# Performance work log

Measured on AMD Instinct MI355X. Metric: run time of the kernel, lower is better.

Reference implementation:

```python
import jax, jax.numpy as jnp
import numpy as np
from jax import lax

DT = jnp.float32
P_DIM = 21
G_VEC = jnp.array([0.0, 0.0, -9.80665], dtype=DT)
# process-noise diag: (omega, acc, b_omega, b_acc, Rot_c_i, t_c_i) x3 each (NumPyIEKF.Parameters defaults)
Q_DIAG = jnp.array([1e-3] * 3 + [1e-2] * 3 + [6e-9] * 3 + [2e-4] * 3 + [1e-9] * 3 + [1e-9] * 3, dtype=DT)
COV_ROT0, COV_V0 = 1e-3, 1e-1
COV_B_OMEGA0, COV_B_ACC0 = 6e-3, 4e-3
COV_ROT_C_I0, COV_T_C_I0 = 1e-6, 5e-3


def _skew(x):
    z = jnp.zeros((), x.dtype)
    return jnp.stack([
        jnp.stack([z, -x[2], x[1]]),
        jnp.stack([x[2], z, -x[0]]),
        jnp.stack([-x[1], x[0], z]),
    ])


def _so3exp(phi):
    # SO(3) exponential (Rodrigues), safe at phi ~ 0 via double-where.
    I3 = jnp.eye(3, dtype=phi.dtype)
    sq = jnp.dot(phi, phi)
    small = sq < 1e-16
    angle = jnp.sqrt(jnp.where(small, 1.0, sq))
    axis = phi / angle
    s, c = jnp.sin(angle), jnp.cos(angle)
    R = c * I3 + (1.0 - c) * jnp.outer(axis, axis) + s * _skew(axis)
    return jnp.where(small, I3 + _skew(phi), R)


def _sen3exp(xi):
    # SE_2(3) exponential: xi is 9-vector [phi, dv_raw, dp_raw]; returns (dR, x) with x[:,0]=dv, x[:,1]=dp.
    phi = xi[:3]
    I3 = jnp.eye(3, dtype=xi.dtype)
    sq = jnp.dot(phi, phi)
    small = sq < 1e-16
    angle = jnp.sqrt(jnp.where(small, 1.0, sq))
    axis = phi / angle
    s, c = jnp.sin(angle), jnp.cos(angle)
    sk = _skew(axis)
    outer = jnp.outer(axis, axis)
    sa = s / angle
    J = sa * I3 + (1.0 - sa) * outer + ((1.0 - c) / angle) * sk
    R = c * I3 + (1.0 - c) * outer + s * sk
    J = jnp.where(small, I3 + 0.5 * _skew(phi), J)
    R = jnp.where(small, I3 + _skew(phi), R)
    x = J @ xi[3:].reshape(2, 3).T  # (3,2)
    return R, x


def _from_rpy(roll, pitch, yaw):
    cr, sr = jnp.cos(roll), jnp.sin(roll)
    cp, sp = jnp.cos(pitch), jnp.sin(pitch)
    cy, sy = jnp.cos(yaw), jnp.sin(yaw)
    z = jnp.zeros((), roll.dtype)
    o = jnp.ones((), roll.dtype)
    rx = jnp.stack([jnp.stack([o, z, z]), jnp.stack([z, cr, -sr]), jnp.stack([z, sr, cr])])
    ry = jnp.stack([jnp.stack([cp, z, sp]), jnp.stack([z, o, z]), jnp.stack([-sp, z, cp])])
    rz = jnp.stack([jnp.stack([cy, -sy, z]), jnp.stack([sy, cy, z]), jnp.stack([z, z, o])])
    return rz @ ry @ rx


def _propagate_cov(P, Rot, v, p, u, dt):
    I3 = jnp.eye(3, dtype=P.dtype)
    v_skew_rot = _skew(v) @ Rot
    p_skew_rot = _skew(p) @ Rot
    F = jnp.zeros((P_DIM, P_DIM), P.dtype)
    F = F.at[3:6, :3].set(_skew(G_VEC))
    F = F.at[6:9, 3:6].set(I3)
    F = F.at[3:6, 12:15].set(-Rot)
    F = F.at[:3, 9:12].set(-Rot)
    F = F.at[3:6, 9:12].set(-v_skew_rot)
    F = F.at[6:9, 9:12].set(-p_skew_rot)
    G = jnp.zeros((P_DIM, 18), P.dtype)
    G = G.at[:3, :3].set(Rot).at[3:6, :3].set(v_skew_rot).at[6:9, :3].set(p_skew_rot)
    G = G.at[3:6, 3:6].set(Rot)
    G = G.at[9:12, 6:9].set(I3).at[12:15, 9:12].set(I3).at[15:18, 12:15].set(I3).at[18:21, 15:18].set(I3)
    F = F * dt
    G = G * dt
    F2 = F @ F
    Phi = jnp.eye(P_DIM, dtype=P.dtype) + F + 0.5 * F2 + (1.0 / 6.0) * (F2 @ F)
    return Phi @ (P + (G * Q_DIAG) @ G.T) @ Phi.T


def _step(carry, inp):
    Rot, v, p, b_omega, b_acc, Rot_c_i, t_c_i, P = carry
    u, dt, mcov = inp
    # ---- propagate ----
    acc = Rot @ (u[3:6] - b_acc) + G_VEC
    v_n = v + acc * dt
    p_n = p + v * dt + 0.5 * acc * dt * dt
    Rot_n = Rot @ _so3exp((u[:3] - b_omega) * dt)
    P_n = _propagate_cov(P, Rot, v, p, u, dt)
    # ---- update: zero lateral/vertical body-velocity pseudo-measurement ----
    Rot_body = Rot_n @ Rot_c_i
    v_imu = Rot_n.T @ v_n
    omega = u[:3] - b_omega
    v_body = Rot_c_i.T @ v_imu + _skew(t_c_i) @ omega
    H = jnp.zeros((2, P_DIM), P.dtype)
    H = H.at[:, 3:6].set(Rot_body.T[1:])
    H = H.at[:, 15:18].set((Rot_c_i.T @ _skew(v_imu))[1:])
    H = H.at[:, 9:12].set(_skew(t_c_i)[1:])
    H = H.at[:, 18:21].set(-_skew(omega)[1:])
    r = -v_body[1:]
    Rm = jnp.diag(mcov)
    S = H @ P_n @ H.T + Rm  # (2,2)
    K = jnp.linalg.solve(S, H @ P_n.T).T  # K = P H^T S^{-1}, (21,2)
    dx = K @ r
    dR, dxi = _sen3exp(dx[:9])
    Rot_u = dR @ Rot_n
    v_u = dR @ v_n + dxi[:, 0]
    p_u = dR @ p_n + dxi[:, 1]
    b_omega_u = b_omega + dx[9:12]
    b_acc_u = b_acc + dx[12:15]
    Rot_c_i_u = _so3exp(dx[15:18]) @ Rot_c_i
    t_c_i_u = t_c_i + dx[18:21]
    I_KH = jnp.eye(P_DIM, dtype=P.dtype) - K @ H
    P_u = I_KH @ P_n @ I_KH.T + K @ Rm @ K.T
    P_u = 0.5 * (P_u + P_u.T)
    carry = (Rot_u, v_u, p_u, b_omega_u, b_acc_u, Rot_c_i_u, t_c_i_u, P_u)
    return carry, (Rot_u, v_u, p_u, b_omega_u, b_acc_u, Rot_c_i_u, t_c_i_u)


def _run_filter(t, u, mc, v_mes, ang0, remat=False):
    dt = t[1:] - t[:-1]
    dtype = u.dtype
    Rot0 = _from_rpy(ang0[0], ang0[1], ang0[2]).astype(dtype)
    v0 = v_mes[0]
    z3 = jnp.zeros(3, dtype)
    I3 = jnp.eye(3, dtype=dtype)
    p_diag = jnp.array(
        [COV_ROT0, COV_ROT0, 0.0, COV_V0, COV_V0, 0.0, 0.0, 0.0, 0.0]
        + [COV_B_OMEGA0] * 3 + [COV_B_ACC0] * 3 + [COV_ROT_C_I0] * 3 + [COV_T_C_I0] * 3,
        dtype=dtype,
    )
    P0 = jnp.diag(p_diag)
    step = jax.checkpoint(_step) if remat else _step
    carry0 = (Rot0, v0, z3, z3, z3, I3, z3, P0)
    _, traj = lax.scan(step, carry0, (u[1:], dt, mc[1:]))
    first = (Rot0, v0, z3, z3, z3, I3, z3)
    return tuple(jnp.concatenate([f[None], tr], axis=0) for f, tr in zip(first, traj))


def setup_inputs() -> dict:
    key = jax.random.key(0)
    N = 40000  # ~6.7 min of 100 Hz IMU
    k1, k2, k3, k4, k5, k6 = jax.random.split(key, 6)
    t = jnp.arange(N, dtype=DT) * 0.01
    gyro = 0.05 * jax.random.normal(k1, (N, 3), dtype=DT)
    accm = jnp.array([0.0, 0.0, 9.80665], dtype=DT) + 0.1 * jax.random.normal(k2, (N, 3), dtype=DT)
    u = jnp.concatenate([gyro, accm], axis=1)
    measurements_covs = 0.01 + jax.random.uniform(k3, (N, 2), dtype=DT)
    v_mes = jax.random.normal(k4, (N, 3), dtype=DT)
    p_mes = jax.random.normal(k5, (N, 3), dtype=DT)
    ang0 = 0.1 * jax.random.normal(k6, (3,), dtype=DT)
    return {"t": t, "u": u, "measurements_covs": measurements_covs, "v_mes": v_mes,
            "p_mes": p_mes, "ang0": ang0, "N": N}


def reference(t, u, measurements_covs, v_mes, p_mes, ang0, N):
    # p_mes is accepted by run()/init_run() but unused (parity with source).
    return _run_filter(t[:N], u[:N], measurements_covs[:N], v_mes[:N], ang0)
```

## Files before the change

kernel.cpp:

```cpp
#include <hip/hip_runtime.h>
#include <math.h>


#define GRAV 9.80665f
#define P24 24
#define PC  12
#define Q0c 0.001f
#define Q1c 0.01f

#define WSYNC() asm volatile("s_waitcnt lgkmcnt(0)" ::: "memory")

__device__ __forceinline__ float sel3f(int r, float a, float b, float c) {
    return (r == 0) ? a : ((r == 1) ? b : c);
}

__device__ __forceinline__ void m3mul_dev(const float* A, const float* B, float* C) {
#pragma unroll
    for (int i = 0; i < 3; ++i) {
#pragma unroll
        for (int j = 0; j < 3; ++j) {
            C[i*3+j] = A[i*3+0]*B[j] + A[i*3+1]*B[3+j] + A[i*3+2]*B[6+j];
        }
    }
}

__device__ __forceinline__ void so3exp_dev(float p0, float p1, float p2, float* R) {
    float sq = p0*p0 + p1*p1 + p2*p2;
    if (sq < 1e-16f) {
        R[0]=1.f;  R[1]=-p2;  R[2]=p1;
        R[3]=p2;   R[4]=1.f;  R[5]=-p0;
        R[6]=-p1;  R[7]=p0;   R[8]=1.f;
    } else {
        float ang = sqrtf(sq);
        float ax=p0/ang, ay=p1/ang, az=p2/ang;
        float s=sinf(ang), c=cosf(ang), o=1.f-c;
        R[0]=c+o*ax*ax;    R[1]=o*ax*ay-s*az; R[2]=o*ax*az+s*ay;
        R[3]=o*ay*ax+s*az; R[4]=c+o*ay*ay;    R[5]=o*ay*az-s*ax;
        R[6]=o*az*ax-s*ay; R[7]=o*az*ay+s*ax; R[8]=c+o*az*az;
    }
}

#define STORE_TRAJ(NIDX)                                                        \
    do {                                                                        \
        if (l < 33) {                                                           \
            float val = Rot[0];                                                 \
            if (l==1) val=Rot[1];  if (l==2) val=Rot[2];                        \
            if (l==3) val=Rot[3];  if (l==4) val=Rot[4];                        \
            if (l==5) val=Rot[5];  if (l==6) val=Rot[6];                        \
            if (l==7) val=Rot[7];  if (l==8) val=Rot[8];                        \
            if (l==9)  val=vv[0];  if (l==10) val=vv[1];  if (l==11) val=vv[2]; \
            if (l==12) val=pp[0];  if (l==13) val=pp[1];  if (l==14) val=pp[2]; \
            if (l==15) val=bw[0];  if (l==16) val=bw[1];  if (l==17) val=bw[2]; \
            if (l==18) val=ba[0];  if (l==19) val=ba[1];  if (l==20) val=ba[2]; \
            if (l==21) val=Rci[0]; if (l==22) val=Rci[1]; if (l==23) val=Rci[2];\
            if (l==24) val=Rci[3]; if (l==25) val=Rci[4]; if (l==26) val=Rci[5];\
            if (l==27) val=Rci[6]; if (l==28) val=Rci[7]; if (l==29) val=Rci[8];\
            if (l==30) val=tci[0]; if (l==31) val=tci[1]; if (l==32) val=tci[2];\
            out[ob + os_ * (NIDX) + orr] = val;                                 \
        }                                                                       \
    } while (0)

__global__ __launch_bounds__(64, 1)
void iekf_scan_kernel(const float* __restrict__ t,
                      const float* __restrict__ u,
                      const float* __restrict__ mc,
                      const float* __restrict__ v_mes,
                      const float* __restrict__ ang0,
                      float* __restrict__ out,
                      const int N)
{
    __shared__ __align__(16) float sRows[10*4];
    __shared__ __align__(16) float sPhiC[21*PC];
    __shared__ __align__(16) float sAT [22*P24];
    __shared__ __align__(16) float sT1 [22*P24];
    __shared__ __align__(16) float sPn [22*P24];
    __shared__ __align__(16) float sPnT[22*P24];
    __shared__ __align__(16) float sHpack[21*4];
    __shared__ __align__(16) float sKpack[21*4];
    __shared__ __align__(16) float sdx[24];

    const int l = (int)threadIdx.x;

    int ei[7], ej[7], wro[7], wco[7];
    bool ev[7];
#pragma unroll
    for (int q = 0; q < 7; ++q) {
        const int e = 64*q + l;
        const bool v = (e < 441);
        const int ii = e / 21;
        const int jj = e - ii*21;
        ev[q] = v;
        ei[q] = v ? ii : 20;
        ej[q] = v ? jj : 20;
        wro[q] = (v ? ii : 21)*P24 + ej[q];
        wco[q] = (v ? jj : 21)*P24 + ei[q];
    }

    float Rot[9], vv[3], pp[3], bw[3], ba[3], Rci[9], tci[3];
    {
        const float roll = ang0[0], pitch = ang0[1], yaw = ang0[2];
        const float cr = cosf(roll),  srl = sinf(roll);
        const float cp = cosf(pitch), spt = sinf(pitch);
        const float cy = cosf(yaw),   syw = sinf(yaw);
        float rx[9] = {1.f,0.f,0.f, 0.f,cr,-srl, 0.f,srl,cr};
        float ry[9] = {cp,0.f,spt, 0.f,1.f,0.f, -spt,0.f,cp};
        float rz[9] = {cy,-syw,0.f, syw,cy,0.f, 0.f,0.f,1.f};
        float tm[9]; m3mul_dev(rz, ry, tm);
        m3mul_dev(tm, rx, Rot);
        vv[0]=v_mes[0]; vv[1]=v_mes[1]; vv[2]=v_mes[2];
#pragma unroll
        for (int c=0;c<3;c++){ pp[c]=0.f; bw[c]=0.f; ba[c]=0.f; tci[c]=0.f; }
        Rci[0]=1.f;Rci[1]=0.f;Rci[2]=0.f;Rci[3]=0.f;Rci[4]=1.f;Rci[5]=0.f;
        Rci[6]=0.f;Rci[7]=0.f;Rci[8]=1.f;
    }

    float Preg[7];
#pragma unroll
    for (int q = 0; q < 7; ++q) {
        float pd = 0.f;
        if (ev[q] && ei[q] == ej[q]) {
            const int ii = ei[q];
            if (ii==0 || ii==1)        pd = 0.001f;
            else if (ii==3 || ii==4)   pd = 0.1f;
            else if (ii>=9  && ii<12)  pd = 0.006f;
            else if (ii>=12 && ii<15)  pd = 0.004f;
            else if (ii>=15 && ii<18)  pd = 1e-6f;
            else if (ii>=18)           pd = 0.005f;
        }
        Preg[q] = pd;
    }

    int ob=0, os_=0, orr=0;
    if (l<33) {
        if (l<9)       { ob = 0;    os_ = 9; orr = l;    }
        else if (l<12) { ob = 9*N;  os_ = 3; orr = l-9;  }
        else if (l<15) { ob = 12*N; os_ = 3; orr = l-12; }
        else if (l<18) { ob = 15*N; os_ = 3; orr = l-15; }
        else if (l<21) { ob = 18*N; os_ = 3; orr = l-18; }
        else if (l<30) { ob = 21*N; os_ = 9; orr = l-21; }
        else           { ob = 30*N; os_ = 3; orr = l-30; }
    }

    STORE_TRAJ(0);

    float t_cur = t[0];

    float tn_c = t[1];
    float uc0,uc1,uc2,uc3,uc4,uc5;
    { const float* un = u + 6; uc0=un[0]; uc1=un[1]; uc2=un[2]; uc3=un[3]; uc4=un[4]; uc5=un[5]; }
    float mcc0 = mc[2], mcc1 = mc[3];

    for (int n = 0; n < N-1; ++n) {
        const int np2 = (n+2 < N) ? (n+2) : (N-1);
        const float tn_n = t[np2];
        float un0,un1,un2,un3,un4,un5;
        { const float* un = u + (size_t)np2*6; un0=un[0]; un1=un[1]; un2=un[2]; un3=un[3]; un4=un[4]; un5=un[5]; }
        const float mcn0 = mc[2*np2], mcn1 = mc[2*np2+1];

        const float dt  = tn_c - t_cur;
        const float dt2 = dt*dt;
        const float u0=uc0,u1=uc1,u2=uc2,u3=uc3,u4=uc4,u5=uc5;
        const float mcv0=mcc0, mcv1=mcc1;

        float Rot_n[9], v_n[3], p_n[3], om[3], M1[9], M2[9];
        om[0]=u0-bw[0]; om[1]=u1-bw[1]; om[2]=u2-bw[2];
        {
            const float ai0=u3-ba[0], ai1=u4-ba[1], ai2=u5-ba[2];
            const float ac0 = Rot[0]*ai0 + Rot[1]*ai1 + Rot[2]*ai2;
            const float ac1 = Rot[3]*ai0 + Rot[4]*ai1 + Rot[5]*ai2;
            const float ac2 = Rot[6]*ai0 + Rot[7]*ai1 + Rot[8]*ai2 - GRAV;
            v_n[0]=vv[0]+ac0*dt; v_n[1]=vv[1]+ac1*dt; v_n[2]=vv[2]+ac2*dt;
            p_n[0]=pp[0]+vv[0]*dt+0.5f*ac0*dt2;
            p_n[1]=pp[1]+vv[1]*dt+0.5f*ac1*dt2;
            p_n[2]=pp[2]+vv[2]*dt+0.5f*ac2*dt2;
            float E[9]; so3exp_dev(om[0]*dt, om[1]*dt, om[2]*dt, E);
            m3mul_dev(Rot, E, Rot_n);
        }
#pragma unroll
        for (int c=0;c<3;c++) {
            M1[0+c] = -vv[2]*Rot[3+c] + vv[1]*Rot[6+c];
            M1[3+c] =  vv[2]*Rot[0+c] - vv[0]*Rot[6+c];
            M1[6+c] = -vv[1]*Rot[0+c] + vv[0]*Rot[3+c];
            M2[0+c] = -pp[2]*Rot[3+c] + pp[1]*Rot[6+c];
            M2[3+c] =  pp[2]*Rot[0+c] - pp[0]*Rot[6+c];
            M2[6+c] = -pp[1]*Rot[0+c] + pp[0]*Rot[3+c];
        }
        const float hdt2 = 0.5f*dt2;
        const float sdt3 = dt*dt2*(1.0f/6.0f);
        const float dtg = dt*GRAV, hg = hdt2*GRAV;

        if (l < 27) {
            const int ri = l/3, c = l - 3*ri;
            const int rr = (ri<3) ? ri : ((ri<6) ? ri-3 : ri-6);
            const float rotv = sel3f(c, sel3f(rr,Rot[0],Rot[3],Rot[6]),
                                        sel3f(rr,Rot[1],Rot[4],Rot[7]),
                                        sel3f(rr,Rot[2],Rot[5],Rot[8]));
            const float m1v  = sel3f(c, sel3f(rr,M1[0],M1[3],M1[6]),
                                        sel3f(rr,M1[1],M1[4],M1[7]),
                                        sel3f(rr,M1[2],M1[5],M1[8]));
            const float m2v  = sel3f(c, sel3f(rr,M2[0],M2[3],M2[6]),
                                        sel3f(rr,M2[1],M2[4],M2[7]),
                                        sel3f(rr,M2[2],M2[5],M2[8]));
            sRows[ri*4 + c] = (ri<3) ? rotv : ((ri<6) ? m1v : m2v);
        }
        if (l < 21) {
            const int j = l, br = j/3, r = j - 3*br;
            float cf[12];
#pragma unroll
            for (int c=0;c<3;c++) {
                const float m0r = sel3f(r, Rot[0+c], Rot[3+c], Rot[6+c]);
                const float m1r = sel3f(r, M1[0+c], M1[3+c], M1[6+c]);
                const float m2r = sel3f(r, M2[0+c], M2[3+c], M2[6+c]);
                const float sgm = sel3f(r, GRAV*Rot[3+c], -GRAV*Rot[0+c], 0.f);
                cf[0+c] = (br==0) ? (-dt*m0r)
                        : (br==1) ? (-dt*m1r - hdt2*sgm)
                        : (br==2) ? (-dt*m2r - hdt2*m1r - sdt3*sgm) : 0.f;
                cf[3+c] = (br==1) ? (-dt*m0r) : (br==2) ? (-hdt2*m0r) : 0.f;
                cf[8+c] = (br==2 && r==c) ? dt : 0.f;
            }
            cf[6] = (br==1) ? ((r==1)? -dtg : 0.f) : (br==2) ? ((r==1)? -hg : 0.f) : 0.f;
            cf[7] = (br==1) ? ((r==0)?  dtg : 0.f) : (br==2) ? ((r==0)?  hg : 0.f) : 0.f;
            cf[11] = 0.f;
            float4 w0; w0.x=cf[0]; w0.y=cf[1]; w0.z=cf[2]; w0.w=cf[3];
            float4 w1; w1.x=cf[4]; w1.y=cf[5]; w1.z=cf[6]; w1.w=cf[7];
            float4 w2; w2.x=cf[8]; w2.y=cf[9]; w2.z=cf[10]; w2.w=cf[11];
            *(float4*)&sPhiC[j*PC+0] = w0;
            *(float4*)&sPhiC[j*PC+4] = w1;
            *(float4*)&sPhiC[j*PC+8] = w2;
        }

        float H0_3,H0_4,H0_5,H1_3,H1_4,H1_5,H0_9,H0_10,H0_11,H1_9,H1_10,H1_11;
        float H0_15,H0_16,H0_17,H1_15,H1_16,H1_17,H0_18,H0_19,H0_20,H1_18,H1_19,H1_20;
        float r0s, r1s;
        {
            float Rb[9]; m3mul_dev(Rot_n, Rci, Rb);
            const float vi0 = Rot_n[0]*v_n[0] + Rot_n[3]*v_n[1] + Rot_n[6]*v_n[2];
            const float vi1 = Rot_n[1]*v_n[0] + Rot_n[4]*v_n[1] + Rot_n[7]*v_n[2];
            const float vi2 = Rot_n[2]*v_n[0] + Rot_n[5]*v_n[1] + Rot_n[8]*v_n[2];
            H0_3 = Rb[1]; H0_4 = Rb[4]; H0_5 = Rb[7];
            H1_3 = Rb[2]; H1_4 = Rb[5]; H1_5 = Rb[8];
            H0_9 = tci[2]; H0_10 = 0.f; H0_11 = -tci[0];
            H1_9 = -tci[1]; H1_10 = tci[0]; H1_11 = 0.f;
            H0_15 =  Rci[4]*vi2 - Rci[7]*vi1;
            H0_16 = -Rci[1]*vi2 + Rci[7]*vi0;
            H0_17 =  Rci[1]*vi1 - Rci[4]*vi0;
            H1_15 =  Rci[5]*vi2 - Rci[8]*vi1;
            H1_16 = -Rci[2]*vi2 + Rci[8]*vi0;
            H1_17 =  Rci[2]*vi1 - Rci[5]*vi0;
            H0_18 = -om[2]; H0_19 = 0.f; H0_20 = om[0];
            H1_18 = om[1];  H1_19 = -om[0]; H1_20 = 0.f;
            const float vb1 = Rci[1]*vi0 + Rci[4]*vi1 + Rci[7]*vi2 + (tci[2]*om[0] - tci[0]*om[2]);
            const float vb2 = Rci[2]*vi0 + Rci[5]*vi1 + Rci[8]*vi2 + (tci[0]*om[1] - tci[1]*om[0]);
            r0s = -vb1; r1s = -vb2;
        }
        WSYNC();

        float Areg[7];
#pragma unroll
        for (int q = 0; q < 7; ++q) {
            float Wij;
            if (q <= 2) {
                const bool gqv = (ei[q] < 9) && (ej[q] < 9);
                const int ra_r = (ei[q] < 9) ? ei[q] : 9;
                const int rb_r = (ej[q] < 9) ? ej[q] : 9;
                const float4 ra = *(const float4*)&sRows[ra_r*4];
                const float4 rb = *(const float4*)&sRows[rb_r*4];
                float w = dt2*Q0c*(ra.x*rb.x + ra.y*rb.y + ra.z*rb.z);
                const int ri = ei[q]-3, rj = ej[q]-3;
                const float ra0=sel3f(ri,Rot[0],Rot[3],Rot[6]), ra1=sel3f(ri,Rot[1],Rot[4],Rot[7]), ra2=sel3f(ri,Rot[2],Rot[5],Rot[8]);
                const float rb0=sel3f(rj,Rot[0],Rot[3],Rot[6]), rb1=sel3f(rj,Rot[1],Rot[4],Rot[7]), rb2=sel3f(rj,Rot[2],Rot[5],Rot[8]);
                const bool q1v = (ri>=0 && ri<3 && rj>=0 && rj<3);
                const float w2 = w + dt2*Q1c*(ra0*rb0 + ra1*rb1 + ra2*rb2);
                w = q1v ? w2 : w;
                Wij = gqv ? w : 0.f;
            } else {
                const bool dg = ev[q] && (ei[q] == ej[q]);
                const float qd = (ei[q]<12) ? 6e-9f : (ei[q]<15) ? 2e-4f : 1e-9f;
                Wij = dg ? dt2*qd : 0.f;
            }
            Areg[q] = Preg[q] + Wij;
            sAT[wco[q]] = Areg[q];
        }
        WSYNC();

        float T1reg[7];
#pragma unroll
        for (int q = 0; q < 7; ++q) {
            float tv = Areg[q];
            if (q <= 2) {
                const int co = ei[q]*PC;
                const float4 c0 = *(const float4*)&sPhiC[co];
                const float4 c1 = *(const float4*)&sPhiC[co+4];
                const float4 c2 = *(const float4*)&sPhiC[co+8];
                const int ro = ej[q]*P24;
                const float4 a0 = *(const float4*)&sAT[ro];
                const float4 a1 = *(const float4*)&sAT[ro+4];
                const float4 a2 = *(const float4*)&sAT[ro+8];
                const float4 a3 = *(const float4*)&sAT[ro+12];
                tv += c1.z*a0.x;
                tv += c1.w*a0.y;
                tv += c2.x*a0.w;
                tv += c2.y*a1.x;
                tv += c2.z*a1.y;
                tv += c0.x*a2.y;
                tv += c0.y*a2.z;
                tv += c0.z*a2.w;
                tv += c0.w*a3.x;
                tv += c1.x*a3.y;
                tv += c1.y*a3.z;
            }
            T1reg[q] = tv;
            sT1[wro[q]] = tv;
        }
        WSYNC();

        float Pnreg[7];
#pragma unroll
        for (int q = 0; q < 7; ++q) {
            const int co = ej[q]*PC;
            const float4 c0 = *(const float4*)&sPhiC[co];
            const float4 c1 = *(const float4*)&sPhiC[co+4];
            const float4 c2 = *(const float4*)&sPhiC[co+8];
            const int ro = ei[q]*P24;
            const float4 t0 = *(const float4*)&sT1[ro];
            const float4 t1 = *(const float4*)&sT1[ro+4];
            const float4 t2 = *(const float4*)&sT1[ro+8];
            const float4 t3 = *(const float4*)&sT1[ro+12];
            float pv = T1reg[q];
            pv += c1.z*t0.x;
            pv += c1.w*t0.y;
            pv += c2.x*t0.w;
            pv += c2.y*t1.x;
            pv += c2.z*t1.y;
            pv += c0.x*t2.y;
            pv += c0.y*t2.z;
            pv += c0.z*t2.w;
            pv += c0.w*t3.x;
            pv += c1.x*t3.y;
            pv += c1.y*t3.z;
            Pnreg[q] = pv;
            sPn [wro[q]] = pv;
            sPnT[wco[q]] = pv;
        }
        WSYNC();

        {
            const int a  = l / 21;
            const int jj = (l < 42) ? (l - 21*a) : 0;
            const int ro = jj*P24;
            const float4 p0 = *(const float4*)&sPnT[ro];
            const float4 p1 = *(const float4*)&sPnT[ro+4];
            const float4 p2 = *(const float4*)&sPnT[ro+8];
            const float4 p3 = *(const float4*)&sPnT[ro+12];
            const float4 p4 = *(const float4*)&sPnT[ro+16];
            const float4 p5 = *(const float4*)&sPnT[ro+20];
            const float4 q0 = *(const float4*)&sPn[ro];
            const float4 q1 = *(const float4*)&sPn[ro+4];
            const float4 q2 = *(const float4*)&sPn[ro+8];
            const float4 q3 = *(const float4*)&sPn[ro+12];
            const float4 q4 = *(const float4*)&sPn[ro+16];
            const float4 q5 = *(const float4*)&sPn[ro+20];
            const bool a0v = (a == 0);
            const float h3  = a0v ? H0_3  : H1_3,  h4  = a0v ? H0_4  : H1_4,  h5  = a0v ? H0_5  : H1_5;
            const float h9  = a0v ? H0_9  : H1_9,  h10 = a0v ? H0_10 : H1_10, h11 = a0v ? H0_11 : H1_11;
            const float h15 = a0v ? H0_15 : H1_15, h16 = a0v ? H0_16 : H1_16, h17 = a0v ? H0_17 : H1_17;
            const float h18 = a0v ? H0_18 : H1_18, h19 = a0v ? H0_19 : H1_19, h20 = a0v ? H0_20 : H1_20;
            float hp = 0.f;
            hp += h3*p0.w;  hp += h4*p1.x;  hp += h5*p1.y;
            hp += h9*p2.y;  hp += h10*p2.z; hp += h11*p2.w;
            hp += h15*p3.w; hp += h16*p4.x; hp += h17*p4.y;
            hp += h18*p4.z; hp += h19*p4.w; hp += h20*p5.x;
            float ht = 0.f;
            ht += h3*q0.w;  ht += h4*q1.x;  ht += h5*q1.y;
            ht += h9*q2.y;  ht += h10*q2.z; ht += h11*q2.w;
            ht += h15*q3.w; ht += h16*q4.x; ht += h17*q4.y;
            ht += h18*q4.z; ht += h19*q4.w; ht += h20*q5.x;
            if (l < 42) {
                sHpack[jj*4 + a]     = hp;
                sHpack[jj*4 + 2 + a] = ht;
            }
        }
        WSYNC();

        {
            const float4 v3  = *(const float4*)&sHpack[3*4];
            const float4 v4  = *(const float4*)&sHpack[4*4];
            const float4 v5  = *(const float4*)&sHpack[5*4];
            const float4 v9  = *(const float4*)&sHpack[9*4];
            const float4 v10 = *(const float4*)&sHpack[10*4];
            const float4 v11 = *(const float4*)&sHpack[11*4];
            const float4 v15 = *(const float4*)&sHpack[15*4];
            const float4 v16 = *(const float4*)&sHpack[16*4];
            const float4 v17 = *(const float4*)&sHpack[17*4];
            const float4 v18 = *(const float4*)&sHpack[18*4];
            const float4 v19 = *(const float4*)&sHpack[19*4];
            const float4 v20 = *(const float4*)&sHpack[20*4];
            float S00 = 0.f, S01 = 0.f, S10 = 0.f, S11 = 0.f;
            S00 += v3.x*H0_3;  S00 += v4.x*H0_4;  S00 += v5.x*H0_5;
            S00 += v9.x*H0_9;  S00 += v10.x*H0_10; S00 += v11.x*H0_11;
            S00 += v15.x*H0_15; S00 += v16.x*H0_16; S00 += v17.x*H0_17;
            S00 += v18.x*H0_18; S00 += v19.x*H0_19; S00 += v20.x*H0_20;
            S01 += v3.x*H1_3;  S01 += v4.x*H1_4;  S01 += v5.x*H1_5;
            S01 += v9.x*H1_9;  S01 += v10.x*H1_10; S01 += v11.x*H1_11;
            S01 += v15.x*H1_15; S01 += v16.x*H1_16; S01 += v17.x*H1_17;
            S01 += v18.x*H1_18; S01 += v19.x*H1_19; S01 += v20.x*H1_20;
            S10 += v3.y*H0_3;  S10 += v4.y*H0_4;  S10 += v5.y*H0_5;
            S10 += v9.y*H0_9;  S10 += v10.y*H0_10; S10 += v11.y*H0_11;
            S10 += v15.y*H0_15; S10 += v16.y*H0_16; S10 += v17.y*H0_17;
            S10 += v18.y*H0_18; S10 += v19.y*H0_19; S10 += v20.y*H0_20;
            S11 += v3.y*H1_3;  S11 += v4.y*H1_4;  S11 += v5.y*H1_5;
            S11 += v9.y*H1_9;  S11 += v10.y*H1_10; S11 += v11.y*H1_11;
            S11 += v15.y*H1_15; S11 += v16.y*H1_16; S11 += v17.y*H1_17;
            S11 += v18.y*H1_18; S11 += v19.y*H1_19; S11 += v20.y*H1_20;
            S00 += mcv0; S11 += mcv1;
            if (l < 21) {
                const float4 own = *(const float4*)&sHpack[l*4];
                const float b0 = own.z, b1 = own.w;
                float x0, x1;
                if (fabsf(S00) >= fabsf(S10)) {
                    const float fac = S10/S00;
                    x1 = (b1 - fac*b0) / (S11 - fac*S01);
                    x0 = (b0 - S01*x1) / S00;
                } else {
                    const float fac = S00/S10;
                    x1 = (b0 - fac*b1) / (S01 - fac*S11);
                    x0 = (b1 - S11*x1) / S10;
                }
                float4 kp; kp.x = x0; kp.y = x1;
                kp.z = S00*x0 + S01*x1;
                kp.w = S10*x0 + S11*x1;
                *(float4*)&sKpack[l*4] = kp;
                sdx[l] = x0*r0s + x1*r1s;
            }
        }
        WSYNC();

#pragma unroll
        for (int q = 0; q < 7; ++q) {
            const float4 Ki = *(const float4*)&sKpack[ei[q]*4];
            const float4 Kj = *(const float4*)&sKpack[ej[q]*4];
            const float4 Hi = *(const float4*)&sHpack[ei[q]*4];
            const float4 Hj = *(const float4*)&sHpack[ej[q]*4];
            const float pn_ji = sPnT[ei[q]*P24 + ej[q]];
            const float puij = Pnreg[q] - (Ki.x*Hj.x + Ki.y*Hj.y) - (Hi.z*Kj.x + Hi.w*Kj.y)
                                        + (Ki.x*Kj.z + Ki.y*Kj.w);
            const float puji = pn_ji   - (Kj.x*Hi.x + Kj.y*Hi.y) - (Hj.z*Ki.x + Hj.w*Ki.y)
                                        + (Kj.x*Ki.z + Kj.y*Ki.w);
            const float pu = 0.5f*(puij + puji);
            Preg[q] = ev[q] ? pu : Preg[q];
        }
        {
            float dxr[21];
#pragma unroll
            for (int q2=0;q2<6;q2++){
                const float4 x = *(const float4*)(&sdx[4*q2]);
                dxr[4*q2] = x.x;
                if (4*q2+1 < 21) dxr[4*q2+1] = x.y;
                if (4*q2+2 < 21) dxr[4*q2+2] = x.z;
                if (4*q2+3 < 21) dxr[4*q2+3] = x.w;
            }
            float dR[9], Jm[9];
            const float q0 = dxr[0], q1 = dxr[1], q2 = dxr[2];
            const float sq = q0*q0 + q1*q1 + q2*q2;
            if (sq < 1e-16f) {
                dR[0]=1.f; dR[1]=-q2; dR[2]=q1;
                dR[3]=q2;  dR[4]=1.f; dR[5]=-q0;
                dR[6]=-q1; dR[7]=q0;  dR[8]=1.f;
                Jm[0]=1.f;      Jm[1]=-0.5f*q2; Jm[2]=0.5f*q1;
                Jm[3]=0.5f*q2;  Jm[4]=1.f;      Jm[5]=-0.5f*q0;
                Jm[6]=-0.5f*q1; Jm[7]=0.5f*q0;  Jm[8]=1.f;
            } else {
                const float ang = sqrtf(sq);
                const float ax=q0/ang, ay=q1/ang, az=q2/ang;
                const float s=sinf(ang), c=cosf(ang), o=1.f-c;
                dR[0]=c+o*ax*ax;    dR[1]=o*ax*ay-s*az; dR[2]=o*ax*az+s*ay;
                dR[3]=o*ay*ax+s*az; dR[4]=c+o*ay*ay;    dR[5]=o*ay*az-s*ax;
                dR[6]=o*az*ax-s*ay; dR[7]=o*az*ay+s*ax; dR[8]=c+o*az*az;
                const float sa  = s/ang;
                const float osa = 1.f - sa;
                const float tt  = o/ang;
                Jm[0]=sa+osa*ax*ax;    Jm[1]=osa*ax*ay-tt*az; Jm[2]=osa*ax*az+tt*ay;
                Jm[3]=osa*ay*ax+tt*az; Jm[4]=sa+osa*ay*ay;    Jm[5]=osa*ay*az-tt*ax;
                Jm[6]=osa*az*ax-tt*ay; Jm[7]=osa*az*ay+tt*ax; Jm[8]=sa+osa*az*az;
            }
            float nR[9]; m3mul_dev(dR, Rot_n, nR);
#pragma unroll
            for (int c=0;c<9;c++) Rot[c] = nR[c];
            const float dv0 = Jm[0]*dxr[3] + Jm[1]*dxr[4] + Jm[2]*dxr[5];
            const float dv1 = Jm[3]*dxr[3] + Jm[4]*dxr[4] + Jm[5]*dxr[5];
            const float dv2 = Jm[6]*dxr[3] + Jm[7]*dxr[4] + Jm[8]*dxr[5];
            const float dp0 = Jm[0]*dxr[6] + Jm[1]*dxr[7] + Jm[2]*dxr[8];
            const float dp1 = Jm[3]*dxr[6] + Jm[4]*dxr[7] + Jm[5]*dxr[8];
            const float dp2 = Jm[6]*dxr[6] + Jm[7]*dxr[7] + Jm[8]*dxr[8];
            const float nv0 = dR[0]*v_n[0] + dR[1]*v_n[1] + dR[2]*v_n[2] + dv0;
            const float nv1 = dR[3]*v_n[0] + dR[4]*v_n[1] + dR[5]*v_n[2] + dv1;
            const float nv2 = dR[6]*v_n[0] + dR[7]*v_n[1] + dR[8]*v_n[2] + dv2;
            const float np0 = dR[0]*p_n[0] + dR[1]*p_n[1] + dR[2]*p_n[2] + dp0;
            const float np1 = dR[3]*p_n[0] + dR[4]*p_n[1] + dR[5]*p_n[2] + dp1;
            const float np2v= dR[6]*p_n[0] + dR[7]*p_n[1] + dR[8]*p_n[2] + dp2;
            vv[0]=nv0; vv[1]=nv1; vv[2]=nv2;
            pp[0]=np0; pp[1]=np1; pp[2]=np2v;
            bw[0]+=dxr[9];  bw[1]+=dxr[10]; bw[2]+=dxr[11];
            ba[0]+=dxr[12]; ba[1]+=dxr[13]; ba[2]+=dxr[14];
            float E2[9]; so3exp_dev(dxr[15], dxr[16], dxr[17], E2);
            float nRc[9]; m3mul_dev(E2, Rci, nRc);
#pragma unroll
            for (int c=0;c<9;c++) Rci[c] = nRc[c];
            tci[0]+=dxr[18]; tci[1]+=dxr[19]; tci[2]+=dxr[20];
        }
        STORE_TRAJ(n+1);

        t_cur = tn_c;
        tn_c  = tn_n;
        uc0=un0; uc1=un1; uc2=un2; uc3=un3; uc4=un4; uc5=un5;
        mcc0=mcn0; mcc1=mcn1;
    }
}

extern "C" void kernel_launch(void* const* d_in, const int* in_sizes, int n_in,
                              void* d_out, int out_size, void* d_ws, size_t ws_size,
                              hipStream_t stream) {
    const float* t     = (const float*)d_in[0];
    const float* u     = (const float*)d_in[1];
    const float* mc    = (const float*)d_in[2];
    const float* v_mes = (const float*)d_in[3];
    const float* ang0  = (const float*)d_in[5];
    float* out = (float*)d_out;
    const int N = in_sizes[0];
    (void)d_ws; (void)ws_size; (void)n_in; (void)out_size;
    iekf_scan_kernel<<<1, 64, 0, stream>>>(t, u, mc, v_mes, ang0, out, N);
}
```

Before: 202.4 ms.

## Switch covariance update to per-thread column ownership in registers

Instead of distributing the 441 covariance entries across 64 threads in 7-element chunks, each of the first 21 threads now owns a full column of P in registers. Phi coefficients are computed inline rather than staged through shared memory, which removes several shared buffers and one barrier stage. Each thread also solves the 2x2 innovation system redundantly, so there is no separate K broadcast pass. The trade-off is that only 21 of 64 lanes do useful work, and each thread needs many more registers for its column arrays and coefficient tables.

```diff
diff --git a/kernel.cpp b/kernel.cpp
--- a/kernel.cpp
+++ b/kernel.cpp
@@ -3,8 +3,7 @@
 
 
 #define GRAV 9.80665f
-#define P24 24
-#define PC  12
+#define PIT 36
 #define Q0c 0.001f
 #define Q1c 0.01f
 
@@ -69,32 +68,17 @@
                       float* __restrict__ out,
                       const int N)
 {
-    __shared__ __align__(16) float sRows[10*4];
-    __shared__ __align__(16) float sPhiC[21*PC];
-    __shared__ __align__(16) float sAT [22*P24];
-    __shared__ __align__(16) float sT1 [22*P24];
-    __shared__ __align__(16) float sPn [22*P24];
-    __shared__ __align__(16) float sPnT[22*P24];
-    __shared__ __align__(16) float sHpack[21*4];
-    __shared__ __align__(16) float sKpack[21*4];
+    __shared__ __align__(16) float sT1[21*PIT];
+    __shared__ __align__(16) float sPT[21*PIT];
+    __shared__ __align__(16) float sHK[21*4];
+    __shared__ __align__(16) float sKK[21*4];
     __shared__ __align__(16) float sdx[24];
 
     const int l = (int)threadIdx.x;
-
-    int ei[7], ej[7], wro[7], wco[7];
-    bool ev[7];
-#pragma unroll
-    for (int q = 0; q < 7; ++q) {
-        const int e = 64*q + l;
-        const bool v = (e < 441);
-        const int ii = e / 21;
-        const int jj = e - ii*21;
-        ev[q] = v;
-        ei[q] = v ? ii : 20;
-        ej[q] = v ? jj : 20;
-        wro[q] = (v ? ii : 21)*P24 + ej[q];
-        wco[q] = (v ? jj : 21)*P24 + ei[q];
-    }
+    const int jc = (l < 21) ? l : 20;
+    const bool own = (l < 21);
+
+    if (l >= 21 && l < 24) sdx[l] = 0.f;
 
     float Rot[9], vv[3], pp[3], bw[3], ba[3], Rci[9], tci[3];
     {
@@ -114,20 +98,17 @@
         Rci[6]=0.f;Rci[7]=0.f;Rci[8]=1.f;
     }
 
-    float Preg[7];
-#pragma unroll
-    for (int q = 0; q < 7; ++q) {
+    float Pcol[21];
+#pragma unroll
+    for (int i=0;i<21;i++){
         float pd = 0.f;
-        if (ev[q] && ei[q] == ej[q]) {
-            const int ii = ei[q];
-            if (ii==0 || ii==1)        pd = 0.001f;
-            else if (ii==3 || ii==4)   pd = 0.1f;
-            else if (ii>=9  && ii<12)  pd = 0.006f;
-            else if (ii>=12 && ii<15)  pd = 0.004f;
-            else if (ii>=15 && ii<18)  pd = 1e-6f;
-            else if (ii>=18)           pd = 0.005f;
-        }
-        Preg[q] = pd;
+        if (i==0 || i==1)        pd = 0.001f;
+        else if (i==3 || i==4)   pd = 0.1f;
+        else if (i>=9  && i<12)  pd = 0.006f;
+        else if (i>=12 && i<15)  pd = 0.004f;
+        else if (i>=15 && i<18)  pd = 1e-6f;
+        else if (i>=18)          pd = 0.005f;
+        Pcol[i] = (own && i==jc) ? pd : 0.f;
     }
 
     int ob=0, os_=0, orr=0;
@@ -188,46 +169,6 @@
         const float hdt2 = 0.5f*dt2;
         const float sdt3 = dt*dt2*(1.0f/6.0f);
         const float dtg = dt*GRAV, hg = hdt2*GRAV;
-
-        if (l < 27) {
-            const int ri = l/3, c = l - 3*ri;
-            const int rr = (ri<3) ? ri : ((ri<6) ? ri-3 : ri-6);
-            const float rotv = sel3f(c, sel3f(rr,Rot[0],Rot[3],Rot[6]),
-                                        sel3f(rr,Rot[1],Rot[4],Rot[7]),
-                                        sel3f(rr,Rot[2],Rot[5],Rot[8]));
-            const float m1v  = sel3f(c, sel3f(rr,M1[0],M1[3],M1[6]),
-                                        sel3f(rr,M1[1],M1[4],M1[7]),
-                                        sel3f(rr,M1[2],M1[5],M1[8]));
-            const float m2v  = sel3f(c, sel3f(rr,M2[0],M2[3],M2[6]),
-                                        sel3f(rr,M2[1],M2[4],M2[7]),
-                                        sel3f(rr,M2[2],M2[5],M2[8]));
-            sRows[ri*4 + c] = (ri<3) ? rotv : ((ri<6) ? m1v : m2v);
-        }
-        if (l < 21) {
-            const int j = l, br = j/3, r = j - 3*br;
-            float cf[12];
-#pragma unroll
-            for (int c=0;c<3;c++) {
-                const float m0r = sel3f(r, Rot[0+c], Rot[3+c], Rot[6+c]);
-                const float m1r = sel3f(r, M1[0+c], M1[3+c], M1[6+c]);
-                const float m2r = sel3f(r, M2[0+c], M2[3+c], M2[6+c]);
-                const float sgm = sel3f(r, GRAV*Rot[3+c], -GRAV*Rot[0+c], 0.f);
-                cf[0+c] = (br==0) ? (-dt*m0r)
-                        : (br==1) ? (-dt*m1r - hdt2*sgm)
-                        : (br==2) ? (-dt*m2r - hdt2*m1r - sdt3*sgm) : 0.f;
-                cf[3+c] = (br==1) ? (-dt*m0r) : (br==2) ? (-hdt2*m0r) : 0.f;
-                cf[8+c] = (br==2 && r==c) ? dt : 0.f;
-            }
-            cf[6] = (br==1) ? ((r==1)? -dtg : 0.f) : (br==2) ? ((r==1)? -hg : 0.f) : 0.f;
-            cf[7] = (br==1) ? ((r==0)?  dtg : 0.f) : (br==2) ? ((r==0)?  hg : 0.f) : 0.f;
-            cf[11] = 0.f;
-            float4 w0; w0.x=cf[0]; w0.y=cf[1]; w0.z=cf[2]; w0.w=cf[3];
-            float4 w1; w1.x=cf[4]; w1.y=cf[5]; w1.z=cf[6]; w1.w=cf[7];
-            float4 w2; w2.x=cf[8]; w2.y=cf[9]; w2.z=cf[10]; w2.w=cf[11];
-            *(float4*)&sPhiC[j*PC+0] = w0;
-            *(float4*)&sPhiC[j*PC+4] = w1;
-            *(float4*)&sPhiC[j*PC+8] = w2;
-        }
 
         float H0_3,H0_4,H0_5,H1_3,H1_4,H1_5,H0_9,H0_10,H0_11,H1_9,H1_10,H1_11;
         float H0_15,H0_16,H0_17,H1_15,H1_16,H1_17,H0_18,H0_19,H0_20,H1_18,H1_19,H1_20;
@@ -253,148 +194,205 @@
             const float vb2 = Rci[2]*vi0 + Rci[5]*vi1 + Rci[8]*vi2 + (tci[0]*om[1] - tci[1]*om[0]);
             r0s = -vb1; r1s = -vb2;
         }
+
+        const int jb = jc/3, rj = jc - 3*jb;
+        float mj0,mj1,mj2;
+        {
+            const float t0 = sel3f(rj,Rot[0],Rot[3],Rot[6]);
+            const float t1 = sel3f(rj,Rot[1],Rot[4],Rot[7]);
+            const float t2 = sel3f(rj,Rot[2],Rot[5],Rot[8]);
+            const float a0 = sel3f(rj,M1[0],M1[3],M1[6]);
+            const float a1 = sel3f(rj,M1[1],M1[4],M1[7]);
+            const float a2 = sel3f(rj,M1[2],M1[5],M1[8]);
+            const float b0 = sel3f(rj,M2[0],M2[3],M2[6]);
+            const float b1 = sel3f(rj,M2[1],M2[4],M2[7]);
+            const float b2 = sel3f(rj,M2[2],M2[5],M2[8]);
+            mj0 = sel3f(jb, t0, a0, b0);
+            mj1 = sel3f(jb, t1, a1, b1);
+            mj2 = sel3f(jb, t2, a2, b2);
+        }
+        const bool jlt9 = (jc < 9);
+        const bool jq1  = (jc >= 3 && jc < 6);
+        const int  rq   = jc - 3;
+        const float rjq0 = sel3f(rq,Rot[0],Rot[3],Rot[6]);
+        const float rjq1 = sel3f(rq,Rot[1],Rot[4],Rot[7]);
+        const float rjq2 = sel3f(rq,Rot[2],Rot[5],Rot[8]);
+
+        float Acol[21];
+#pragma unroll
+        for (int i=0;i<21;i++){
+            float W;
+            if (i < 9) {
+                const float mi0 = (i<3)?Rot[i*3+0] : (i<6)?M1[(i-3)*3+0] : M2[(i-6)*3+0];
+                const float mi1 = (i<3)?Rot[i*3+1] : (i<6)?M1[(i-3)*3+1] : M2[(i-6)*3+1];
+                const float mi2 = (i<3)?Rot[i*3+2] : (i<6)?M1[(i-3)*3+2] : M2[(i-6)*3+2];
+                float w = dt2*Q0c*(mi0*mj0 + mi1*mj1 + mi2*mj2);
+                if (i>=3 && i<6) {
+                    const float ri0 = Rot[(i-3)*3+0], ri1 = Rot[(i-3)*3+1], ri2 = Rot[(i-3)*3+2];
+                    const float w2 = w + dt2*Q1c*(ri0*rjq0 + ri1*rjq1 + ri2*rjq2);
+                    w = jq1 ? w2 : w;
+                }
+                W = jlt9 ? w : 0.f;
+            } else {
+                const float qd = (i<12)?6e-9f : (i<15)?2e-4f : 1e-9f;
+                W = (own && i==jc) ? dt2*qd : 0.f;
+            }
+            Acol[i] = Pcol[i] + W;
+        }
+
+        float cbw[9][3], cba[9][3];
+#pragma unroll
+        for (int i=0;i<9;i++){
+            const int br=i/3, r=i-3*br;
+#pragma unroll
+            for (int c=0;c<3;c++){
+                const float m0r = (r==0)?Rot[c]:(r==1)?Rot[3+c]:Rot[6+c];
+                const float m1r = (r==0)?M1[c]:(r==1)?M1[3+c]:M1[6+c];
+                const float m2r = (r==0)?M2[c]:(r==1)?M2[3+c]:M2[6+c];
+                const float sgm = (r==0)? GRAV*Rot[3+c] : (r==1)? -GRAV*Rot[0+c] : 0.f;
+                cbw[i][c] = (br==0)? (-dt*m0r) : (br==1)? (-dt*m1r - hdt2*sgm)
+                                               : (-dt*m2r - hdt2*m1r - sdt3*sgm);
+                cba[i][c] = (br==0)? 0.f : (br==1)? (-dt*m0r) : (-hdt2*m0r);
+            }
+        }
+
+        float T1col[21];
+#pragma unroll
+        for (int i=0;i<21;i++){
+            if (i < 9) {
+                const int br=i/3, r=i-3*br;
+                const float ca0 = (br==1)? ((r==1)? -dtg:0.f) : (br==2)? ((r==1)? -hg:0.f) : 0.f;
+                const float ca1 = (br==1)? ((r==0)?  dtg:0.f) : (br==2)? ((r==0)?  hg:0.f) : 0.f;
+                const float cv0 = (br==2 && r==0)? dt : 0.f;
+                const float cv1 = (br==2 && r==1)? dt : 0.f;
+                const float cv2 = (br==2 && r==2)? dt : 0.f;
+                float tv = Acol[i];
+                tv += ca0*Acol[0];
+                tv += ca1*Acol[1];
+                tv += cv0*Acol[3];
+                tv += cv1*Acol[4];
+                tv += cv2*Acol[5];
+                tv += cbw[i][0]*Acol[9];
+                tv += cbw[i][1]*Acol[10];
+                tv += cbw[i][2]*Acol[11];
+                tv += cba[i][0]*Acol[12];
+                tv += cba[i][1]*Acol[13];
+                tv += cba[i][2]*Acol[14];
+                T1col[i] = tv;
+            } else {
+                T1col[i] = Acol[i];
+            }
+        }
+
+        if (own) {
+#pragma unroll
+            for (int i=0;i<21;i++) sT1[i*PIT + l] = T1col[i];
+        }
         WSYNC();
-
-        float Areg[7];
-#pragma unroll
-        for (int q = 0; q < 7; ++q) {
-            float Wij;
-            if (q <= 2) {
-                const bool gqv = (ei[q] < 9) && (ej[q] < 9);
-                const int ra_r = (ei[q] < 9) ? ei[q] : 9;
-                const int rb_r = (ej[q] < 9) ? ej[q] : 9;
-                const float4 ra = *(const float4*)&sRows[ra_r*4];
-                const float4 rb = *(const float4*)&sRows[rb_r*4];
-                float w = dt2*Q0c*(ra.x*rb.x + ra.y*rb.y + ra.z*rb.z);
-                const int ri = ei[q]-3, rj = ej[q]-3;
-                const float ra0=sel3f(ri,Rot[0],Rot[3],Rot[6]), ra1=sel3f(ri,Rot[1],Rot[4],Rot[7]), ra2=sel3f(ri,Rot[2],Rot[5],Rot[8]);
-                const float rb0=sel3f(rj,Rot[0],Rot[3],Rot[6]), rb1=sel3f(rj,Rot[1],Rot[4],Rot[7]), rb2=sel3f(rj,Rot[2],Rot[5],Rot[8]);
-                const bool q1v = (ri>=0 && ri<3 && rj>=0 && rj<3);
-                const float w2 = w + dt2*Q1c*(ra0*rb0 + ra1*rb1 + ra2*rb2);
-                w = q1v ? w2 : w;
-                Wij = gqv ? w : 0.f;
+        float T1row[21];
+        {
+            const float* rp = &sT1[jc*PIT];
+            const float4 a0 = *(const float4*)(rp+0);
+            const float4 a1 = *(const float4*)(rp+4);
+            const float4 a2 = *(const float4*)(rp+8);
+            const float4 a3 = *(const float4*)(rp+12);
+            const float4 a4 = *(const float4*)(rp+16);
+            const float4 a5 = *(const float4*)(rp+20);
+            T1row[0]=a0.x;  T1row[1]=a0.y;  T1row[2]=a0.z;  T1row[3]=a0.w;
+            T1row[4]=a1.x;  T1row[5]=a1.y;  T1row[6]=a1.z;  T1row[7]=a1.w;
+            T1row[8]=a2.x;  T1row[9]=a2.y;  T1row[10]=a2.z; T1row[11]=a2.w;
+            T1row[12]=a3.x; T1row[13]=a3.y; T1row[14]=a3.z; T1row[15]=a3.w;
+            T1row[16]=a4.x; T1row[17]=a4.y; T1row[18]=a4.z; T1row[19]=a4.w;
+            T1row[20]=a5.x;
+        }
+
+        float Pnrow[21];
+#pragma unroll
+        for (int m=0;m<21;m++){
+            if (m < 9) {
+                const int br=m/3, r=m-3*br;
+                const float ca0 = (br==1)? ((r==1)? -dtg:0.f) : (br==2)? ((r==1)? -hg:0.f) : 0.f;
+                const float ca1 = (br==1)? ((r==0)?  dtg:0.f) : (br==2)? ((r==0)?  hg:0.f) : 0.f;
+                const float cv0 = (br==2 && r==0)? dt : 0.f;
+                const float cv1 = (br==2 && r==1)? dt : 0.f;
+                const float cv2 = (br==2 && r==2)? dt : 0.f;
+                float pv = T1row[m];
+                pv += ca0*T1row[0];
+                pv += ca1*T1row[1];
+                pv += cv0*T1row[3];
+                pv += cv1*T1row[4];
+                pv += cv2*T1row[5];
+                pv += cbw[m][0]*T1row[9];
+                pv += cbw[m][1]*T1row[10];
+                pv += cbw[m][2]*T1row[11];
+                pv += cba[m][0]*T1row[12];
+                pv += cba[m][1]*T1row[13];
+                pv += cba[m][2]*T1row[14];
+                Pnrow[m] = pv;
             } else {
-                const bool dg = ev[q] && (ei[q] == ej[q]);
-                const float qd = (ei[q]<12) ? 6e-9f : (ei[q]<15) ? 2e-4f : 1e-9f;
-                Wij = dg ? dt2*qd : 0.f;
-            }
-            Areg[q] = Preg[q] + Wij;
-            sAT[wco[q]] = Areg[q];
+                Pnrow[m] = T1row[m];
+            }
+        }
+
+        if (own) {
+#pragma unroll
+            for (int m=0;m<21;m++) sPT[m*PIT + l] = Pnrow[m];
         }
         WSYNC();
-
-        float T1reg[7];
-#pragma unroll
-        for (int q = 0; q < 7; ++q) {
-            float tv = Areg[q];
-            if (q <= 2) {
-                const int co = ei[q]*PC;
-                const float4 c0 = *(const float4*)&sPhiC[co];
-                const float4 c1 = *(const float4*)&sPhiC[co+4];
-                const float4 c2 = *(const float4*)&sPhiC[co+8];
-                const int ro = ej[q]*P24;
-                const float4 a0 = *(const float4*)&sAT[ro];
-                const float4 a1 = *(const float4*)&sAT[ro+4];
-                const float4 a2 = *(const float4*)&sAT[ro+8];
-                const float4 a3 = *(const float4*)&sAT[ro+12];
-                tv += c1.z*a0.x;
-                tv += c1.w*a0.y;
-                tv += c2.x*a0.w;
-                tv += c2.y*a1.x;
-                tv += c2.z*a1.y;
-                tv += c0.x*a2.y;
-                tv += c0.y*a2.z;
-                tv += c0.z*a2.w;
-                tv += c0.w*a3.x;
-                tv += c1.x*a3.y;
-                tv += c1.y*a3.z;
-            }
-            T1reg[q] = tv;
-            sT1[wro[q]] = tv;
+        float Pncol[21];
+        {
+            const float* rp = &sPT[jc*PIT];
+            const float4 a0 = *(const float4*)(rp+0);
+            const float4 a1 = *(const float4*)(rp+4);
+            const float4 a2 = *(const float4*)(rp+8);
+            const float4 a3 = *(const float4*)(rp+12);
+            const float4 a4 = *(const float4*)(rp+16);
+            const float4 a5 = *(const float4*)(rp+20);
+            Pncol[0]=a0.x;  Pncol[1]=a0.y;  Pncol[2]=a0.z;  Pncol[3]=a0.w;
+            Pncol[4]=a1.x;  Pncol[5]=a1.y;  Pncol[6]=a1.z;  Pncol[7]=a1.w;
+            Pncol[8]=a2.x;  Pncol[9]=a2.y;  Pncol[10]=a2.z; Pncol[11]=a2.w;
+            Pncol[12]=a3.x; Pncol[13]=a3.y; Pncol[14]=a3.z; Pncol[15]=a3.w;
+            Pncol[16]=a4.x; Pncol[17]=a4.y; Pncol[18]=a4.z; Pncol[19]=a4.w;
+            Pncol[20]=a5.x;
+        }
+
+        float hp0=0.f, hp1=0.f, ht0=0.f, ht1=0.f;
+        hp0 += H0_3*Pncol[3];   hp0 += H0_4*Pncol[4];   hp0 += H0_5*Pncol[5];
+        hp0 += H0_9*Pncol[9];   hp0 += H0_10*Pncol[10]; hp0 += H0_11*Pncol[11];
+        hp0 += H0_15*Pncol[15]; hp0 += H0_16*Pncol[16]; hp0 += H0_17*Pncol[17];
+        hp0 += H0_18*Pncol[18]; hp0 += H0_19*Pncol[19]; hp0 += H0_20*Pncol[20];
+        hp1 += H1_3*Pncol[3];   hp1 += H1_4*Pncol[4];   hp1 += H1_5*Pncol[5];
+        hp1 += H1_9*Pncol[9];   hp1 += H1_10*Pncol[10]; hp1 += H1_11*Pncol[11];
+        hp1 += H1_15*Pncol[15]; hp1 += H1_16*Pncol[16]; hp1 += H1_17*Pncol[17];
+        hp1 += H1_18*Pncol[18]; hp1 += H1_19*Pncol[19]; hp1 += H1_20*Pncol[20];
+        ht0 += H0_3*Pnrow[3];   ht0 += H0_4*Pnrow[4];   ht0 += H0_5*Pnrow[5];
+        ht0 += H0_9*Pnrow[9];   ht0 += H0_10*Pnrow[10]; ht0 += H0_11*Pnrow[11];
+        ht0 += H0_15*Pnrow[15]; ht0 += H0_16*Pnrow[16]; ht0 += H0_17*Pnrow[17];
+        ht0 += H0_18*Pnrow[18]; ht0 += H0_19*Pnrow[19]; ht0 += H0_20*Pnrow[20];
+        ht1 += H1_3*Pnrow[3];   ht1 += H1_4*Pnrow[4];   ht1 += H1_5*Pnrow[5];
+        ht1 += H1_9*Pnrow[9];   ht1 += H1_10*Pnrow[10]; ht1 += H1_11*Pnrow[11];
+        ht1 += H1_15*Pnrow[15]; ht1 += H1_16*Pnrow[16]; ht1 += H1_17*Pnrow[17];
+        ht1 += H1_18*Pnrow[18]; ht1 += H1_19*Pnrow[19]; ht1 += H1_20*Pnrow[20];
+        if (own) {
+            float4 hk; hk.x=hp0; hk.y=hp1; hk.z=ht0; hk.w=ht1;
+            *(float4*)&sHK[l*4] = hk;
         }
         WSYNC();
 
-        float Pnreg[7];
-#pragma unroll
-        for (int q = 0; q < 7; ++q) {
-            const int co = ej[q]*PC;
-            const float4 c0 = *(const float4*)&sPhiC[co];
-            const float4 c1 = *(const float4*)&sPhiC[co+4];
-            const float4 c2 = *(const float4*)&sPhiC[co+8];
-            const int ro = ei[q]*P24;
-            const float4 t0 = *(const float4*)&sT1[ro];
-            const float4 t1 = *(const float4*)&sT1[ro+4];
-            const float4 t2 = *(const float4*)&sT1[ro+8];
-            const float4 t3 = *(const float4*)&sT1[ro+12];
-            float pv = T1reg[q];
-            pv += c1.z*t0.x;
-            pv += c1.w*t0.y;
-            pv += c2.x*t0.w;
-            pv += c2.y*t1.x;
-            pv += c2.z*t1.y;
-            pv += c0.x*t2.y;
-            pv += c0.y*t2.z;
-            pv += c0.z*t2.w;
-            pv += c0.w*t3.x;
-            pv += c1.x*t3.y;
-            pv += c1.y*t3.z;
-            Pnreg[q] = pv;
-            sPn [wro[q]] = pv;
-            sPnT[wco[q]] = pv;
-        }
-        WSYNC();
-
-        {
-            const int a  = l / 21;
-            const int jj = (l < 42) ? (l - 21*a) : 0;
-            const int ro = jj*P24;
-            const float4 p0 = *(const float4*)&sPnT[ro];
-            const float4 p1 = *(const float4*)&sPnT[ro+4];
-            const float4 p2 = *(const float4*)&sPnT[ro+8];
-            const float4 p3 = *(const float4*)&sPnT[ro+12];
-            const float4 p4 = *(const float4*)&sPnT[ro+16];
-            const float4 p5 = *(const float4*)&sPnT[ro+20];
-            const float4 q0 = *(const float4*)&sPn[ro];
-            const float4 q1 = *(const float4*)&sPn[ro+4];
-            const float4 q2 = *(const float4*)&sPn[ro+8];
-            const float4 q3 = *(const float4*)&sPn[ro+12];
-            const float4 q4 = *(const float4*)&sPn[ro+16];
-            const float4 q5 = *(const float4*)&sPn[ro+20];
-            const bool a0v = (a == 0);
-            const float h3  = a0v ? H0_3  : H1_3,  h4  = a0v ? H0_4  : H1_4,  h5  = a0v ? H0_5  : H1_5;
-            const float h9  = a0v ? H0_9  : H1_9,  h10 = a0v ? H0_10 : H1_10, h11 = a0v ? H0_11 : H1_11;
-            const float h15 = a0v ? H0_15 : H1_15, h16 = a0v ? H0_16 : H1_16, h17 = a0v ? H0_17 : H1_17;
-            const float h18 = a0v ? H0_18 : H1_18, h19 = a0v ? H0_19 : H1_19, h20 = a0v ? H0_20 : H1_20;
-            float hp = 0.f;
-            hp += h3*p0.w;  hp += h4*p1.x;  hp += h5*p1.y;
-            hp += h9*p2.y;  hp += h10*p2.z; hp += h11*p2.w;
-            hp += h15*p3.w; hp += h16*p4.x; hp += h17*p4.y;
-            hp += h18*p4.z; hp += h19*p4.w; hp += h20*p5.x;
-            float ht = 0.f;
-            ht += h3*q0.w;  ht += h4*q1.x;  ht += h5*q1.y;
-            ht += h9*q2.y;  ht += h10*q2.z; ht += h11*q2.w;
-            ht += h15*q3.w; ht += h16*q4.x; ht += h17*q4.y;
-            ht += h18*q4.z; ht += h19*q4.w; ht += h20*q5.x;
-            if (l < 42) {
-                sHpack[jj*4 + a]     = hp;
-                sHpack[jj*4 + 2 + a] = ht;
-            }
-        }
-        WSYNC();
-
-        {
-            const float4 v3  = *(const float4*)&sHpack[3*4];
-            const float4 v4  = *(const float4*)&sHpack[4*4];
-            const float4 v5  = *(const float4*)&sHpack[5*4];
-            const float4 v9  = *(const float4*)&sHpack[9*4];
-            const float4 v10 = *(const float4*)&sHpack[10*4];
-            const float4 v11 = *(const float4*)&sHpack[11*4];
-            const float4 v15 = *(const float4*)&sHpack[15*4];
-            const float4 v16 = *(const float4*)&sHpack[16*4];
-            const float4 v17 = *(const float4*)&sHpack[17*4];
-            const float4 v18 = *(const float4*)&sHpack[18*4];
-            const float4 v19 = *(const float4*)&sHpack[19*4];
-            const float4 v20 = *(const float4*)&sHpack[20*4];
+        float x0, x1, ks0, ks1;
+        {
+            const float4 v3  = *(const float4*)&sHK[3*4];
+            const float4 v4  = *(const float4*)&sHK[4*4];
+            const float4 v5  = *(const float4*)&sHK[5*4];
+            const float4 v9  = *(const float4*)&sHK[9*4];
+            const float4 v10 = *(const float4*)&sHK[10*4];
+            const float4 v11 = *(const float4*)&sHK[11*4];
+            const float4 v15 = *(const float4*)&sHK[15*4];
+            const float4 v16 = *(const float4*)&sHK[16*4];
+            const float4 v17 = *(const float4*)&sHK[17*4];
+            const float4 v18 = *(const float4*)&sHK[18*4];
+            const float4 v19 = *(const float4*)&sHK[19*4];
+            const float4 v20 = *(const float4*)&sHK[20*4];
             float S00 = 0.f, S01 = 0.f, S10 = 0.f, S11 = 0.f;
             S00 += v3.x*H0_3;  S00 += v4.x*H0_4;  S00 += v5.x*H0_5;
             S00 += v9.x*H0_9;  S00 += v10.x*H0_10; S00 += v11.x*H0_11;
@@ -413,42 +411,37 @@
             S11 += v15.y*H1_15; S11 += v16.y*H1_16; S11 += v17.y*H1_17;
             S11 += v18.y*H1_18; S11 += v19.y*H1_19; S11 += v20.y*H1_20;
             S00 += mcv0; S11 += mcv1;
-            if (l < 21) {
-                const float4 own = *(const float4*)&sHpack[l*4];
-                const float b0 = own.z, b1 = own.w;
-                float x0, x1;
-                if (fabsf(S00) >= fabsf(S10)) {
-                    const float fac = S10/S00;
-                    x1 = (b1 - fac*b0) / (S11 - fac*S01);
-                    x0 = (b0 - S01*x1) / S00;
-                } else {
-                    const float fac = S00/S10;
-                    x1 = (b0 - fac*b1) / (S01 - fac*S11);
-                    x0 = (b1 - S11*x1) / S10;
-                }
-                float4 kp; kp.x = x0; kp.y = x1;
-                kp.z = S00*x0 + S01*x1;
-                kp.w = S10*x0 + S11*x1;
-                *(float4*)&sKpack[l*4] = kp;
+            const float b0 = ht0, b1 = ht1;
+            if (fabsf(S00) >= fabsf(S10)) {
+                const float fac = S10/S00;
+                x1 = (b1 - fac*b0) / (S11 - fac*S01);
+                x0 = (b0 - S01*x1) / S00;
+            } else {
+                const float fac = S00/S10;
+                x1 = (b0 - fac*b1) / (S01 - fac*S11);
+                x0 = (b1 - S11*x1) / S10;
+            }
+            ks0 = S00*x0 + S01*x1;
+            ks1 = S10*x0 + S11*x1;
+            if (own) {
+                float4 kp; kp.x=x0; kp.y=x1; kp.z=ks0; kp.w=ks1;
+                *(float4*)&sKK[l*4] = kp;
                 sdx[l] = x0*r0s + x1*r1s;
             }
         }
         WSYNC();
 
 #pragma unroll
-        for (int q = 0; q < 7; ++q) {
-            const float4 Ki = *(const float4*)&sKpack[ei[q]*4];
-            const float4 Kj = *(const float4*)&sKpack[ej[q]*4];
-            const float4 Hi = *(const float4*)&sHpack[ei[q]*4];
-            const float4 Hj = *(const float4*)&sHpack[ej[q]*4];
-            const float pn_ji = sPnT[ei[q]*P24 + ej[q]];
-            const float puij = Pnreg[q] - (Ki.x*Hj.x + Ki.y*Hj.y) - (Hi.z*Kj.x + Hi.w*Kj.y)
-                                        + (Ki.x*Kj.z + Ki.y*Kj.w);
-            const float puji = pn_ji   - (Kj.x*Hi.x + Kj.y*Hi.y) - (Hj.z*Ki.x + Hj.w*Ki.y)
-                                        + (Kj.x*Ki.z + Kj.y*Ki.w);
-            const float pu = 0.5f*(puij + puji);
-            Preg[q] = ev[q] ? pu : Preg[q];
-        }
+        for (int i=0;i<21;i++){
+            const float4 Ki = *(const float4*)&sKK[i*4];
+            const float4 Hi = *(const float4*)&sHK[i*4];
+            const float puij = Pncol[i] - (Ki.x*hp0 + Ki.y*hp1) - (Hi.z*x0 + Hi.w*x1)
+                                        + (Ki.x*ks0 + Ki.y*ks1);
+            const float puji = Pnrow[i] - (x0*Hi.x + x1*Hi.y) - (ht0*Ki.x + ht1*Ki.y)
+                                        + (x0*Ki.z + x1*Ki.w);
+            Pcol[i] = 0.5f*(puij + puji);
+        }
+
         {
             float dxr[21];
 #pragma unroll
```

New measurement: 166.5 ms. -17.7%, faster.
